# Performance work log

Hardware: AMD Instinct MI355X
Metric: run time of the kernel (lower is better)

Reference implementation:

```python
import jax, jax.numpy as jnp
import numpy as np

N = 100_000   # nodes
E = 1_200_000 # edges
D = 64        # in_dim
H = 64        # hidden_dim
B = 1000      # graphs in batch
C = 10        # num_classes
TOPO = 64     # topo_dim
BN_EPS = 1e-5


def setup_inputs() -> dict:
    key = jax.random.key(0)
    ks = jax.random.split(key, 24)
    x = jax.random.normal(ks[0], (N, D), dtype=jnp.float32)
    edge_index = jax.random.randint(ks[1], (2, E), 0, N, dtype=jnp.int32)
    # sorted graph ids; force last id = B-1 so batch.max()+1 == B (matches torch path)
    batch = jnp.sort(jax.random.randint(ks[2], (N,), 0, B, dtype=jnp.int32)).at[-1].set(B - 1)
    topo = jax.random.normal(ks[3], (B, TOPO), dtype=jnp.float32)
    s = 0.05
    return {
        "x": x, "edge_index": edge_index, "batch": batch, "topo": topo,
        # conv1 MLP: Linear(D,H) -> BN(H) -> ReLU -> Linear(H,H) -> ReLU
        "W1a": jax.random.normal(ks[4], (D, H)) * s, "b1a": jax.random.normal(ks[5], (H,)) * s,
        "g1": 1.0 + jax.random.normal(ks[6], (H,)) * s, "be1": jax.random.normal(ks[7], (H,)) * s,
        "m1": jax.random.normal(ks[8], (H,)) * s, "v1": 0.5 + jax.random.uniform(ks[9], (H,)),
        "W1b": jax.random.normal(ks[10], (H, H)) * s, "b1b": jax.random.normal(ks[11], (H,)) * s,
        # conv2 MLP: Linear(H,H) -> BN(H) -> ReLU
        "W2": jax.random.normal(ks[12], (H, H)) * s, "b2": jax.random.normal(ks[13], (H,)) * s,
        "g2": 1.0 + jax.random.normal(ks[14], (H,)) * s, "be2": jax.random.normal(ks[15], (H,)) * s,
        "m2": jax.random.normal(ks[16], (H,)) * s, "v2": 0.5 + jax.random.uniform(ks[17], (H,)),
        # topo_net: Linear(TOPO,H) -> ReLU
        "Wt": jax.random.normal(ks[18], (TOPO, H)) * s, "bt": jax.random.normal(ks[19], (H,)) * s,
        # classifier: Linear(2H, C)
        "Wc": jax.random.normal(ks[20], (2 * H, C)) * s, "bc": jax.random.normal(ks[21], (C,)) * s,
    }


def _bn_eval(v, g, b, m, var):
    # BatchNorm1d in eval mode: affine with running stats
    return g * (v - m) * jax.lax.rsqrt(var + BN_EPS) + b


def _gin_agg(h, src, dst):
    # GINConv (eps=0): (1+eps)*x_i + sum_{j->i} x_j ; scatter-add over dst
    return h + jax.ops.segment_sum(h[src], dst, num_segments=N)


def reference(x, edge_index, batch, topo,
              W1a, b1a, g1, be1, m1, v1, W1b, b1b,
              W2, b2, g2, be2, m2, v2, Wt, bt, Wc, bc):
    src, dst = edge_index[0], edge_index[1]
    # conv1: MLP(agg(x)) = Lin -> BN -> ReLU -> Lin -> ReLU; outer relu from forward
    h = _gin_agg(x, src, dst)                              # [N, D]
    h = jax.nn.relu(_bn_eval(h @ W1a + b1a, g1, be1, m1, v1))
    h = jax.nn.relu(h @ W1b + b1b)                         # [N, H]
    h = jax.nn.relu(h)                                     # F.relu(conv1(...))
    # dropout(p=0.5) is identity in eval mode
    # conv2: Lin -> BN -> ReLU, then outer relu
    h = _gin_agg(h, src, dst)                              # [N, H]
    h = jax.nn.relu(_bn_eval(h @ W2 + b2, g2, be2, m2, v2))
    h = jax.nn.relu(h)
    # global_add_pool: sum nodes per graph
    x_struct = jax.ops.segment_sum(h, batch, num_segments=B)   # [B, H]
    # topo already [B, TOPO] => all reshape/pad branches are no-ops
    x_topo = jax.nn.relu(topo @ Wt + bt)                   # [B, H]
    combined = jnp.concatenate([x_struct, x_topo], axis=1) # [B, 2H]
    return combined @ Wc + bc                              # [B, C]
```

## Files before the change

kernel.cpp:

```cpp
#include <hip/hip_runtime.h>

#define N_NODES 100000
#define N_EDGES 1200000
#define DIM     64
#define BGRAPHS 1000
#define NCLASS  10
#define BN_EPS  1e-5f

#define NBUCK   256
#define NPB     391
#define MAGIC   10984572u
#define CHUNK   8192
#define NBLK_P  147
#define BCAP    8192
#define NB_G    1563

typedef __attribute__((ext_vector_type(8))) short   bfx8;
typedef __attribute__((ext_vector_type(4))) float   f32x4;
typedef __attribute__((ext_vector_type(8))) unsigned short u16x8;

__device__ __forceinline__ unsigned short f2bf(float f) {
    unsigned u = __builtin_bit_cast(unsigned, f);
    unsigned r = (u + 0x7FFFu + ((u >> 16) & 1u)) >> 16;
    return (unsigned short)r;
}
__device__ __forceinline__ float bf2f(unsigned short h) {
    unsigned u = ((unsigned)h) << 16;
    return __builtin_bit_cast(float, u);
}

__device__ __forceinline__ bfx8 load_wfrag(const float* __restrict__ W, int kt, int q, int col) {
    bfx8 f;
    #pragma unroll
    for (int j = 0; j < 8; ++j)
        f[j] = (short)f2bf(W[(kt * 32 + q * 8 + j) * 64 + col]);
    return f;
}

__global__ __launch_bounds__(256) void prep_kernel(
    const float* __restrict__ x,
    const float* __restrict__ W1a, unsigned short* __restrict__ y0,
    float* __restrict__ xs,
    const float* __restrict__ W1b, const float* __restrict__ W2,
    unsigned short* __restrict__ w1bp, unsigned short* __restrict__ w2p,
    const float* __restrict__ b1a, const float* __restrict__ g1,
    const float* __restrict__ be1, const float* __restrict__ m1,
    const float* __restrict__ v1,
    const float* __restrict__ b2,  const float* __restrict__ g2,
    const float* __restrict__ be2, const float* __restrict__ m2,
    const float* __restrict__ v2,
    float* __restrict__ AB, int* __restrict__ cursor) {
    __shared__ unsigned short outt[4][16 * 64];
    int t = threadIdx.x;
    if (blockIdx.x < NB_G) {
        int g = blockIdx.x;
        if (g < (BGRAPHS * DIM) / 256) xs[g * 256 + t] = 0.f;
        int w = t >> 6, lane = t & 63;
        int m = lane & 15, q = lane >> 4;
        int row0 = g * 64 + w * 16;

        bfx8 wa[4][2];
        #pragma unroll
        for (int nt = 0; nt < 4; ++nt)
            #pragma unroll
            for (int kt = 0; kt < 2; ++kt)
                wa[nt][kt] = load_wfrag(W1a, kt, q, nt * 16 + m);

        int rowA = row0 + m;
        if (rowA > N_NODES - 1) rowA = N_NODES - 1;
        const float* xp = x + (long long)rowA * 64;
        bfx8 a0, a1;
        #pragma unroll
        for (int j = 0; j < 8; ++j) {
            a0[j] = (short)f2bf(xp[q * 8 + j]);
            a1[j] = (short)f2bf(xp[32 + q * 8 + j]);
        }
        f32x4 acc[4];
        #pragma unroll
        for (int nt = 0; nt < 4; ++nt) {
            acc[nt] = (f32x4){0.f, 0.f, 0.f, 0.f};
            acc[nt] = __builtin_amdgcn_mfma_f32_16x16x32_bf16(a0, wa[nt][0], acc[nt], 0, 0, 0);
            acc[nt] = __builtin_amdgcn_mfma_f32_16x16x32_bf16(a1, wa[nt][1], acc[nt], 0, 0, 0);
        }
        #pragma unroll
        for (int nt = 0; nt < 4; ++nt)
            #pragma unroll
            for (int r = 0; r < 4; ++r)
                outt[w][(q * 4 + r) * 64 + nt * 16 + m] = f2bf(acc[nt][r]);
        __syncthreads();
        #pragma unroll
        for (int i = lane; i < 128; i += 64) {
            int rr = i >> 3, cc = i & 7;
            int rg = row0 + rr;
            if (rg < N_NODES)
                ((float4*)y0)[(long long)rg * 8 + cc] = *(const float4*)&outt[w][rr * 64 + cc * 8];
        }
    } else {
        cursor[t] = t * BCAP;
        const float* Ws[2] = {W1b, W2};
        unsigned short* Wp[2] = {w1bp, w2p};
        #pragma unroll
        for (int wsel = 0; wsel < 2; ++wsel) {
            const float* W = Ws[wsel];
            #pragma unroll
            for (int r = 0; r < 2; ++r) {
                int e = r * 256 + t;
                int kt = e >> 8, q = (e >> 6) & 3, col = e & 63;
                u16x8 o;
                #pragma unroll
                for (int j = 0; j < 8; ++j)
                    o[j] = f2bf(W[(kt * 32 + q * 8 + j) * 64 + col]);
                ((u16x8*)Wp[wsel])[e] = o;
            }
        }
        if (t < 64) {
            float s1 = g1[t] * rsqrtf(v1[t] + BN_EPS);
            AB[t]       = s1;
            AB[64 + t]  = b1a[t] * s1 + (be1[t] - m1[t] * s1);
            float s2 = g2[t] * rsqrtf(v2[t] + BN_EPS);
            AB[128 + t] = s2;
            AB[192 + t] = b2[t] * s2 + (be2[t] - m2[t] * s2);
        }
    }
}

__global__ __launch_bounds__(256) void part_kernel(const int* __restrict__ ei,
                                                   int* __restrict__ cursor,
                                                   int* __restrict__ srcbuf,
                                                   unsigned short* __restrict__ dstlbuf) {
    __shared__ int cnt[NBUCK];
    __shared__ int cur[NBUCK];
    int t = threadIdx.x, blk = blockIdx.x;
    cnt[t] = 0;
    __syncthreads();
    int e0 = blk * CHUNK;
    for (int i = t; i < CHUNK; i += 256) {
        int e = e0 + i;
        if (e >= N_EDGES) break;
        unsigned d = (unsigned)ei[N_EDGES + e];
        atomicAdd(&cnt[__umulhi(d, MAGIC)], 1);
    }
    __syncthreads();
    cur[t] = atomicAdd(&cursor[t], cnt[t]);
    __syncthreads();
    for (int i = t; i < CHUNK; i += 256) {
        int e = e0 + i;
        if (e >= N_EDGES) break;
        unsigned d = (unsigned)ei[N_EDGES + e];
        int sv = ei[e];
        int b = __umulhi(d, MAGIC);
        int pos = atomicAdd(&cur[b], 1);
        srcbuf[pos] = sv;
        dstlbuf[pos] = (unsigned short)(d - b * NPB);
    }
}

__global__ __launch_bounds__(256) void refine_kernel(const int* __restrict__ srcbuf,
                                                     const unsigned short* __restrict__ dstlbuf,
                                                     const int* __restrict__ cursor,
                                                     int* __restrict__ csr_src,
                                                     int* __restrict__ rowptr,
                                                     int* __restrict__ rowend) {
    __shared__ int cnt[NPB + 1];
    __shared__ int cur[NPB + 1];
    __shared__ int tmp[256];
    __shared__ int outb[BCAP];
    int t = threadIdx.x, b = blockIdx.x;
    int beg = b * BCAP;
    int end = cursor[b];

    for (int i = t; i < NPB + 1; i += 256) cnt[i] = 0;
    __syncthreads();
    for (int i = beg + t; i < end; i += 256)
        atomicAdd(&cnt[dstlbuf[i]], 1);
    __syncthreads();

    int i0 = 2 * t, i1 = 2 * t + 1;
    int v0 = (i0 < NPB) ? cnt[i0] : 0;
    int v1 = (i1 < NPB) ? cnt[i1] : 0;
    int s = v0 + v1;
    tmp[t] = s;
    __syncthreads();
    for (int off = 1; off < 256; off <<= 1) {
        int a = (t >= off) ? tmp[t - off] : 0;
        __syncthreads();
        tmp[t] += a;
        __syncthreads();
    }
    int excl = tmp[t] - s;
    if (i0 < NPB) cur[i0] = excl;
    if (i1 < NPB) cur[i1] = excl + v0;
    {
        int g0 = b * NPB + i0;
        if (i0 < NPB && g0 < N_NODES) {
            rowptr[g0] = beg + excl;
            rowend[g0] = beg + excl + v0;
        }
        int g1 = b * NPB + i1;
        if (i1 < NPB && g1 < N_NODES) {
            rowptr[g1] = beg + excl + v0;
            rowend[g1] = beg + excl + v0 + v1;
        }
    }
    __syncthreads();

    for (int i = beg + t; i < end; i += 256) {
        int dl = dstlbuf[i];
        int pos = atomicAdd(&cur[dl], 1);
        if (pos < BCAP) outb[pos] = srcbuf[i];
    }
    __syncthreads();

    int nb = end - beg; if (nb > BCAP) nb = BCAP;
    for (int i = t; i < nb; i += 256) csr_src[beg + i] = outb[i];
}

__global__ __launch_bounds__(256) void gather_mlp1_kernel(
    const unsigned short* __restrict__ feat,
    const int* __restrict__ rowptr, const int* __restrict__ rowend,
    const int* __restrict__ csr_src,
    const float* __restrict__ AB,
    const unsigned short* __restrict__ w1bp, const float* __restrict__ b1b,
    const unsigned short* __restrict__ w2p,
    unsigned short* __restrict__ y2) {
    __shared__ unsigned short h1t[32 * 72];
    __shared__ unsigned short h2t[32 * 72];
    __shared__ unsigned short outt[32 * 64];

    int t = threadIdx.x;
    int nl = t >> 3, q8 = t & 7;
    int node = blockIdx.x * 32 + nl;
    const u16x8* f8 = (const u16x8*)feat;
    {
        u16x8 sv = f8[(long long)node * 8 + q8];
        float acc[8];
        #pragma unroll
        for (int j = 0; j < 8; ++j) acc[j] = bf2f(sv[j]);
        int beg = rowptr[node], end = rowend[node];
        int k = beg;
        int sn = (k < end) ? csr_src[k] : 0;
        while (k < end) {
            int sc = sn;
            ++k;
            if (k < end) sn = csr_src[k];
            u16x8 v = f8[(long long)sc * 8 + q8];
            #pragma unroll
            for (int j = 0; j < 8; ++j) acc[j] += bf2f(v[j]);
        }
        #pragma unroll
        for (int j = 0; j < 8; ++j) {
            int c = q8 * 8 + j;
            h1t[nl * 72 + c] = f2bf(fmaxf(acc[j] * AB[c] + AB[64 + c], 0.f));
        }
    }
    __syncthreads();

    int w = t >> 6, lane = t & 63;
    int m = lane & 15, q = lane >> 4;
    int rt = w >> 1;
    int c0 = (w & 1) * 2;

    const bfx8* wbp = (const bfx8*)w1bp;
    const bfx8* wcp = (const bfx8*)w2p;

    {
        const bfx8* hp = (const bfx8*)&h1t[(rt * 16 + m) * 72];
        bfx8 a0 = hp[q];
        bfx8 a1 = hp[4 + q];
        #pragma unroll
        for (int ci = 0; ci < 2; ++ci) {
            int ct = c0 + ci;
            bfx8 w0 = wbp[(0 * 4 + q) * 64 + ct * 16 + m];
            bfx8 w1 = wbp[(1 * 4 + q) * 64 + ct * 16 + m];
            f32x4 acc = (f32x4){0.f, 0.f, 0.f, 0.f};
            acc = __builtin_amdgcn_mfma_f32_16x16x32_bf16(a0, w0, acc, 0, 0, 0);
            acc = __builtin_amdgcn_mfma_f32_16x16x32_bf16(a1, w1, acc, 0, 0, 0);
            float bb = b1b[ct * 16 + m];
            #pragma unroll
            for (int r = 0; r < 4; ++r)
                h2t[(rt * 16 + q * 4 + r) * 72 + ct * 16 + m] = f2bf(fmaxf(acc[r] + bb, 0.f));
        }
    }
    __syncthreads();

    {
        const bfx8* hp = (const bfx8*)&h2t[(rt * 16 + m) * 72];
        bfx8 a0 = hp[q];
        bfx8 a1 = hp[4 + q];
        #pragma unroll
        for (int ci = 0; ci < 2; ++ci) {
            int ct = c0 + ci;
            bfx8 w0 = wcp[(0 * 4 + q) * 64 + ct * 16 + m];
            bfx8 w1 = wcp[(1 * 4 + q) * 64 + ct * 16 + m];
            f32x4 acc = (f32x4){0.f, 0.f, 0.f, 0.f};
            acc = __builtin_amdgcn_mfma_f32_16x16x32_bf16(a0, w0, acc, 0, 0, 0);
            acc = __builtin_amdgcn_mfma_f32_16x16x32_bf16(a1, w1, acc, 0, 0, 0);
            #pragma unroll
            for (int r = 0; r < 4; ++r)
                outt[(rt * 16 + q * 4 + r) * 64 + ct * 16 + m] = f2bf(acc[r]);
        }
    }
    __syncthreads();

    int rr = t >> 3, cc = t & 7;
    ((float4*)y2)[((long long)blockIdx.x * 32 + rr) * 8 + cc] =
        *(const float4*)&outt[rr * 64 + cc * 8];
}

__global__ __launch_bounds__(256) void gather_pool_kernel(
    const unsigned short* __restrict__ feat,
    const int* __restrict__ rowptr, const int* __restrict__ rowend,
    const int* __restrict__ csr_src,
    const float* __restrict__ AB, const int* __restrict__ batch,
    float* __restrict__ xs) {
    __shared__ float h4[32 * 65];
    __shared__ int bts[32];
    int t = threadIdx.x;
    int nl = t >> 3;
    int q = t & 7;
    int node = blockIdx.x * 32 + nl;
    if (t < 32) bts[t] = batch[blockIdx.x * 32 + t];
    const u16x8* f8 = (const u16x8*)feat;
    u16x8 sv = f8[(long long)node * 8 + q];
    float acc[8];
    #pragma unroll
    for (int j = 0; j < 8; ++j) acc[j] = bf2f(sv[j]);
    int beg = rowptr[node], end = rowend[node];
    int k = beg;
    int sn = (k < end) ? csr_src[k] : 0;
    while (k < end) {
        int sc = sn;
        ++k;
        if (k < end) sn = csr_src[k];
        u16x8 v = f8[(long long)sc * 8 + q];
        #pragma unroll
        for (int j = 0; j < 8; ++j) acc[j] += bf2f(v[j]);
    }
    #pragma unroll
    for (int j = 0; j < 8; ++j) {
        int c = q * 8 + j;
        h4[nl * 65 + c] = fmaxf(acc[j] * AB[128 + c] + AB[192 + c], 0.f);
    }
    __syncthreads();

    int col = t & 63;
    int r0 = (t >> 6) * 8;
    int cb = bts[r0];
    float cur = 0.f;
    #pragma unroll
    for (int r = 0; r < 8; ++r) {
        int b = bts[r0 + r];
        if (b != cb) {
            unsafeAtomicAdd(&xs[cb * 64 + col], cur);
            cb = b;
            cur = 0.f;
        }
        cur += h4[(r0 + r) * 65 + col];
    }
    unsafeAtomicAdd(&xs[cb * 64 + col], cur);
}

__global__ __launch_bounds__(64) void head_kernel(
    const float* __restrict__ xs, const float* __restrict__ topo,
    const float* __restrict__ Wt, const float* __restrict__ bt,
    const float* __restrict__ Wc, const float* __restrict__ bc,
    float* __restrict__ out) {
    __shared__ float trow[64];
    __shared__ float comb[128];
    int b = blockIdx.x;
    int h = threadIdx.x;
    trow[h] = topo[b * 64 + h];
    __syncthreads();
    float acc = bt[h];
    #pragma unroll
    for (int k = 0; k < 64; ++k) acc += trow[k] * Wt[k * 64 + h];
    comb[h] = xs[b * 64 + h];
    comb[64 + h] = fmaxf(acc, 0.f);
    __syncthreads();
    if (h < NCLASS) {
        float o = bc[h];
        #pragma unroll
        for (int k = 0; k < 128; ++k) o += comb[k] * Wc[k * NCLASS + h];
        out[b * NCLASS + h] = o;
    }
}

extern "C" void kernel_launch(void* const* d_in, const int* in_sizes, int n_in,
                              void* d_out, int out_size, void* d_ws, size_t ws_size,
                              hipStream_t stream) {
    const float* x     = (const float*)d_in[0];
    const int*   ei    = (const int*)d_in[1];
    const int*   batch = (const int*)d_in[2];
    const float* topo  = (const float*)d_in[3];
    const float* W1a   = (const float*)d_in[4];
    const float* b1a   = (const float*)d_in[5];
    const float* g1    = (const float*)d_in[6];
    const float* be1   = (const float*)d_in[7];
    const float* m1    = (const float*)d_in[8];
    const float* v1    = (const float*)d_in[9];
    const float* W1b   = (const float*)d_in[10];
    const float* b1b   = (const float*)d_in[11];
    const float* W2    = (const float*)d_in[12];
    const float* b2    = (const float*)d_in[13];
    const float* g2    = (const float*)d_in[14];
    const float* be2   = (const float*)d_in[15];
    const float* m2    = (const float*)d_in[16];
    const float* v2    = (const float*)d_in[17];
    const float* Wt    = (const float*)d_in[18];
    const float* bt    = (const float*)d_in[19];
    const float* Wc    = (const float*)d_in[20];
    const float* bc    = (const float*)d_in[21];
    float* out = (float*)d_out;

    char* p = (char*)d_ws;
    unsigned short* y0   = (unsigned short*)p; p += (size_t)N_NODES * DIM * 2;
    unsigned short* y2b  = (unsigned short*)p; p += (size_t)N_NODES * DIM * 2;
    float* xs      = (float*)p; p += (size_t)BGRAPHS * DIM * 4;
    int*   rowptr  = (int*)p;   p += (size_t)(N_NODES + 16) * 4;
    int*   rowend  = (int*)p;   p += (size_t)(N_NODES + 16) * 4;
    int*   cursor  = (int*)p;   p += 1024;
    unsigned short* w1bp = (unsigned short*)p; p += 512 * 16;
    unsigned short* w2p  = (unsigned short*)p; p += 512 * 16;
    float* AB      = (float*)p; p += 256 * 4;
    int*   srcbuf  = (int*)p;   p += (size_t)NBUCK * BCAP * 4;
    unsigned short* dstlbuf = (unsigned short*)p; p += (size_t)NBUCK * BCAP * 2;
    int*   csr_src = (int*)p;

    prep_kernel<<<NB_G + 1, 256, 0, stream>>>(
        x, W1a, y0, xs, W1b, W2, w1bp, w2p,
        b1a, g1, be1, m1, v1, b2, g2, be2, m2, v2, AB, cursor);
    part_kernel<<<NBLK_P, 256, 0, stream>>>(ei, cursor, srcbuf, dstlbuf);
    refine_kernel<<<NBUCK, 256, 0, stream>>>(srcbuf, dstlbuf, cursor, csr_src, rowptr, rowend);
    gather_mlp1_kernel<<<N_NODES / 32, 256, 0, stream>>>(
        y0, rowptr, rowend, csr_src, AB, w1bp, b1b, w2p, y2b);
    gather_pool_kernel<<<N_NODES / 32, 256, 0, stream>>>(
        y2b, rowptr, rowend, csr_src, AB, batch, xs);
    head_kernel<<<BGRAPHS, 64, 0, stream>>>(xs, topo, Wt, bt, Wc, bc, out);
}
```

Baseline: 225.5 us.

## Stage partitioned edges in LDS and write contiguous packed int2 records

```diff
diff --git a/kernel.cpp b/kernel.cpp
--- a/kernel.cpp
+++ b/kernel.cpp
@@ -126,37 +126,53 @@
 
 __global__ __launch_bounds__(256) void part_kernel(const int* __restrict__ ei,
                                                    int* __restrict__ cursor,
-                                                   int* __restrict__ srcbuf,
-                                                   unsigned short* __restrict__ dstlbuf) {
+                                                   int2* __restrict__ ebuf) {
     __shared__ int cnt[NBUCK];
     __shared__ int cur[NBUCK];
+    __shared__ int goff[NBUCK];
+    __shared__ int tmp[256];
+    __shared__ int2 outb[CHUNK];
     int t = threadIdx.x, blk = blockIdx.x;
+    int e0 = blk * CHUNK;
+    int nE = N_EDGES - e0; if (nE > CHUNK) nE = CHUNK;
+
     cnt[t] = 0;
     __syncthreads();
-    int e0 = blk * CHUNK;
-    for (int i = t; i < CHUNK; i += 256) {
-        int e = e0 + i;
-        if (e >= N_EDGES) break;
-        unsigned d = (unsigned)ei[N_EDGES + e];
+    for (int i = t; i < nE; i += 256) {
+        unsigned d = (unsigned)ei[N_EDGES + e0 + i];
         atomicAdd(&cnt[__umulhi(d, MAGIC)], 1);
     }
     __syncthreads();
-    cur[t] = atomicAdd(&cursor[t], cnt[t]);
-    __syncthreads();
-    for (int i = t; i < CHUNK; i += 256) {
-        int e = e0 + i;
-        if (e >= N_EDGES) break;
-        unsigned d = (unsigned)ei[N_EDGES + e];
-        int sv = ei[e];
-        int b = __umulhi(d, MAGIC);
-        int pos = atomicAdd(&cur[b], 1);
-        srcbuf[pos] = sv;
-        dstlbuf[pos] = (unsigned short)(d - b * NPB);
-    }
-}
-
-__global__ __launch_bounds__(256) void refine_kernel(const int* __restrict__ srcbuf,
-                                                     const unsigned short* __restrict__ dstlbuf,
+    int s = cnt[t];
+    tmp[t] = s;
+    __syncthreads();
+    for (int off = 1; off < 256; off <<= 1) {
+        int a = (t >= off) ? tmp[t - off] : 0;
+        __syncthreads();
+        tmp[t] += a;
+        __syncthreads();
+    }
+    int lbase = tmp[t] - s;
+    int gbase = atomicAdd(&cursor[t], s);
+    cur[t] = lbase;
+    goff[t] = gbase - lbase;
+    __syncthreads();
+    for (int i = t; i < nE; i += 256) {
+        int d = ei[N_EDGES + e0 + i];
+        int sv = ei[e0 + i];
+        int b = __umulhi((unsigned)d, MAGIC);
+        int p = atomicAdd(&cur[b], 1);
+        outb[p] = (int2){sv, d};
+    }
+    __syncthreads();
+    for (int i = t; i < nE; i += 256) {
+        int2 rec = outb[i];
+        int b = __umulhi((unsigned)rec.y, MAGIC);
+        ebuf[goff[b] + i] = rec;
+    }
+}
+
+__global__ __launch_bounds__(256) void refine_kernel(const int2* __restrict__ ebuf,
                                                      const int* __restrict__ cursor,
                                                      int* __restrict__ csr_src,
                                                      int* __restrict__ rowptr,
@@ -168,11 +184,12 @@
     int t = threadIdx.x, b = blockIdx.x;
     int beg = b * BCAP;
     int end = cursor[b];
+    int dbase = b * NPB;
 
     for (int i = t; i < NPB + 1; i += 256) cnt[i] = 0;
     __syncthreads();
     for (int i = beg + t; i < end; i += 256)
-        atomicAdd(&cnt[dstlbuf[i]], 1);
+        atomicAdd(&cnt[ebuf[i].y - dbase], 1);
     __syncthreads();
 
     int i0 = 2 * t, i1 = 2 * t + 1;
@@ -191,12 +208,12 @@
     if (i0 < NPB) cur[i0] = excl;
     if (i1 < NPB) cur[i1] = excl + v0;
     {
-        int g0 = b * NPB + i0;
+        int g0 = dbase + i0;
         if (i0 < NPB && g0 < N_NODES) {
             rowptr[g0] = beg + excl;
             rowend[g0] = beg + excl + v0;
         }
-        int g1 = b * NPB + i1;
+        int g1 = dbase + i1;
         if (i1 < NPB && g1 < N_NODES) {
             rowptr[g1] = beg + excl + v0;
             rowend[g1] = beg + excl + v0 + v1;
@@ -205,9 +222,10 @@
     __syncthreads();
 
     for (int i = beg + t; i < end; i += 256) {
-        int dl = dstlbuf[i];
+        int2 rec = ebuf[i];
+        int dl = rec.y - dbase;
         int pos = atomicAdd(&cur[dl], 1);
-        if (pos < BCAP) outb[pos] = srcbuf[i];
+        if (pos < BCAP) outb[pos] = rec.x;
     }
     __syncthreads();
 
@@ -422,15 +440,14 @@
     unsigned short* w1bp = (unsigned short*)p; p += 512 * 16;
     unsigned short* w2p  = (unsigned short*)p; p += 512 * 16;
     float* AB      = (float*)p; p += 256 * 4;
-    int*   srcbuf  = (int*)p;   p += (size_t)NBUCK * BCAP * 4;
-    unsigned short* dstlbuf = (unsigned short*)p; p += (size_t)NBUCK * BCAP * 2;
+    int2*  ebuf    = (int2*)p;  p += (size_t)NBUCK * BCAP * 8;
     int*   csr_src = (int*)p;
 
     prep_kernel<<<NB_G + 1, 256, 0, stream>>>(
         x, W1a, y0, xs, W1b, W2, w1bp, w2p,
         b1a, g1, be1, m1, v1, b2, g2, be2, m2, v2, AB, cursor);
-    part_kernel<<<NBLK_P, 256, 0, stream>>>(ei, cursor, srcbuf, dstlbuf);
-    refine_kernel<<<NBUCK, 256, 0, stream>>>(srcbuf, dstlbuf, cursor, csr_src, rowptr, rowend);
+    part_kernel<<<NBLK_P, 256, 0, stream>>>(ei, cursor, ebuf);
+    refine_kernel<<<NBUCK, 256, 0, stream>>>(ebuf, cursor, csr_src, rowptr, rowend);
     gather_mlp1_kernel<<<N_NODES / 32, 256, 0, stream>>>(
         y0, rowptr, rowend, csr_src, AB, w1bp, b1b, w2p, y2b);
     gather_pool_kernel<<<N_NODES / 32, 256, 0, stream>>>(
```

New measurement: 214.3 us. 5.0% less time.
